# Performance work log

Measured on AMD Instinct MI355X. Metric: run time of the kernel, lower is better.

Reference implementation:

```python
import jax, jax.numpy as jnp
import numpy as np

B, T, U, L, C = 2048, 100, 512, 3, 10


def setup_inputs() -> dict:
    key = jax.random.key(0)
    ks = jax.random.split(key, 2 + 3 * L + 2)
    x = jax.random.normal(ks[0], (B, T, 1), dtype=jnp.float32)
    mask = jax.random.randint(ks[1], (B, T), 0, 2) > 0
    inp = {"x": x, "mask": mask}
    in_dim = 1
    s = 2
    for l in range(L):
        # Keras LSTM kernel layout: gates ordered [i, f, g(candidate), o]
        inp[f"W{l}"] = jax.random.normal(ks[s], (in_dim, 4 * U), dtype=jnp.float32) * 0.05
        inp[f"U{l}"] = jax.random.normal(ks[s + 1], (U, 4 * U), dtype=jnp.float32) * 0.05
        b = np.zeros((4 * U,), dtype=np.float32)
        b[U:2 * U] = 1.0  # unit_forget_bias (Keras default)
        inp[f"b{l}"] = jnp.asarray(b)
        in_dim = U
        s += 2
    inp["Wd"] = jax.random.normal(ks[s], (U, C), dtype=jnp.float32) * 0.05
    inp["bd"] = jnp.zeros((C,), dtype=jnp.float32)
    return inp


def _lstm_step(x_t, h, c, W, Uw, b):
    z = x_t @ W + h @ Uw + b  # [B, 4U]
    i, f, g, o = jnp.split(z, 4, axis=-1)
    i = jax.nn.sigmoid(i)
    f = jax.nn.sigmoid(f)
    g = jnp.tanh(g)
    o = jax.nn.sigmoid(o)
    c_new = f * c + i * g
    h_new = o * jnp.tanh(c_new)
    return h_new, c_new


def reference(x, mask, W0, U0, b0, W1, U1, b1, W2, U2, b2, Wd, bd):
    params = [(W0, U0, b0), (W1, U1, b1), (W2, U2, b2)]
    xt = jnp.swapaxes(x, 0, 1)        # [T, B, 1]
    mt = jnp.swapaxes(mask, 0, 1)     # [T, B]
    Bsz = x.shape[0]
    init = tuple((jnp.zeros((Bsz, U), x.dtype), jnp.zeros((Bsz, U), x.dtype)) for _ in range(L))

    def scan_fn(carry, inp_t):
        x_t, m_t = inp_t
        m = m_t[:, None]  # [B, 1]
        new_states = []
        layer_in = x_t
        for (h, c), (W, Uw, b) in zip(carry, params):
            h_new, c_new = _lstm_step(layer_in, h, c, W, Uw, b)
            # Keras mask semantics: masked steps carry state/output forward
            h_new = jnp.where(m, h_new, h)
            c_new = jnp.where(m, c_new, c)
            new_states.append((h_new, c_new))
            layer_in = h_new
        return tuple(new_states), None

    final, _ = jax.lax.scan(scan_fn, init, (xt, mt))
    h_top = final[-1][0]  # [B, U]
    logits = h_top @ Wd + bd
    return jax.nn.softmax(logits, axis=-1)
```

## Files before the change

### kernel.cpp

```cpp
#include <hip/hip_runtime.h>
#include <cstdint>
#include <cstddef>

#define B_   2048
#define T_   100
#define U_   512
#define NG_  2048
#define C_   10


typedef __attribute__((ext_vector_type(8))) short   short8;
typedef __attribute__((ext_vector_type(4))) float   floatx4;
typedef unsigned short ushort_t;

__device__ inline ushort_t f2bf(float f){
  unsigned u = __float_as_uint(f);
  unsigned r = (u + 0x7FFFu + ((u >> 16) & 1u)) >> 16;
  return (ushort_t)r;
}
__device__ inline float bf2f(ushort_t b){ return __uint_as_float(((unsigned)b) << 16); }

__device__ inline float sigm(float x){ return 1.0f / (1.0f + __expf(-x)); }
__device__ inline float tanh_fast(float x){
  float a = fabsf(x);
  float e = __expf(-2.0f * a);
  float r = (1.0f - e) / (1.0f + e);
  return copysignf(r, x);
}

__device__ inline int orig_col(int p){
  int Tt  = p >> 7;
  int loc = p & 127;
  int half = loc >> 6;
  int loc2 = loc & 63;
  int gate = loc2 >> 4;
  int uu   = (half << 4) | (loc2 & 15);
  return gate * U_ + Tt * 32 + uu;
}

__device__ inline size_t hidx(int b, int u){
  return (((size_t)(b >> 4) * 64 + (size_t)(u >> 3)) * 16 + (b & 15)) * 8 + (u & 7);
}

#define AS1(p) ((const __attribute__((address_space(1))) void*)(p))
#define AS3(p) ((__attribute__((address_space(3))) void*)(p))

__global__ void convert_weights(
    const float* __restrict__ W0, const float* __restrict__ U0, const float* __restrict__ b0,
    const float* __restrict__ W1, const float* __restrict__ U1, const float* __restrict__ b1,
    const float* __restrict__ W2, const float* __restrict__ U2, const float* __restrict__ b2,
    ushort_t* __restrict__ Bt0, ushort_t* __restrict__ Bt1, ushort_t* __restrict__ Bt2,
    float* __restrict__ W0p, float* __restrict__ biasp)
{
  const int N0 = NG_ * 512;
  const int N1 = NG_ * 1024;
  const int total = N0 + 2 * N1 + NG_ + 3 * NG_;
  int idx = blockIdx.x * 256 + threadIdx.x;
  if (idx >= total) return;

  if (idx < N0){
    int p = idx >> 9, k = idx & 511;
    Bt0[idx] = f2bf(U0[(size_t)k * NG_ + orig_col(p)]);
  } else if (idx < N0 + N1){
    int j = idx - N0; int p = j >> 10, k = j & 1023;
    int oc = orig_col(p);
    float v = (k < 512) ? W1[(size_t)k * NG_ + oc] : U1[(size_t)(k - 512) * NG_ + oc];
    Bt1[j] = f2bf(v);
  } else if (idx < N0 + 2 * N1){
    int j = idx - N0 - N1; int p = j >> 10, k = j & 1023;
    int oc = orig_col(p);
    float v = (k < 512) ? W2[(size_t)k * NG_ + oc] : U2[(size_t)(k - 512) * NG_ + oc];
    Bt2[j] = f2bf(v);
  } else if (idx < N0 + 2 * N1 + NG_){
    int p = idx - N0 - 2 * N1;
    W0p[p] = W0[orig_col(p)];
  } else {
    int j = idx - N0 - 2 * N1 - NG_;
    int l = j >> 11, p = j & 2047;
    const float* bs = (l == 0) ? b0 : (l == 1) ? b1 : b2;
    biasp[j] = bs[orig_col(p)];
  }
}

template<int LAYER>
__device__ __forceinline__ void do_task(
    const ushort_t* __restrict__ A0,
    const ushort_t* __restrict__ A1,
    const ushort_t* __restrict__ Bt,
    const float* __restrict__ biasp,
    const float* __restrict__ W0p,
    const float* __restrict__ x,
    const int* __restrict__ mask,
    float* __restrict__ cbuf,
    const ushort_t* __restrict__ hprev,
    ushort_t* __restrict__ hout,
    int t, int mt, int nt,
    ushort_t* tB)
{
  constexpr int NPHASE = (LAYER == 0) ? 1 : 2;
  constexpr bool IS_L0 = (LAYER == 0);
  constexpr int K  = NPHASE * 512;
  constexpr int NK = NPHASE * 8;

  const int tid  = threadIdx.x;
  const int wv   = tid >> 6;
  const int lane = tid & 63;
  const int qd   = lane >> 4;
  const int l16  = lane & 15;
  const int wave_m = wv >> 1;
  const int wave_n = wv & 1;
  const int m0 = mt * 128, n0 = nt * 128;

  int srow[4], scol[4];
  #pragma unroll
  for (int cc = 0; cc < 4; ++cc){
    int i = cc * 256 + tid;
    srow[cc] = i >> 3;
    scol[cc] = ((i & 7) + (i >> 3)) & 7;
  }

  int boff[2][4];
  #pragma unroll
  for (int ks = 0; ks < 2; ++ks){
    #pragma unroll
    for (int w = 0; w < 4; ++w){
      int Rb = wave_n * 64 + w * 16 + l16;
      int q  = ks * 4 + qd;
      boff[ks][w] = Rb * 64 + ((q - Rb) & 7) * 8;
    }
  }

  size_t abase[4];
  #pragma unroll
  for (int wm = 0; wm < 4; ++wm)
    abase[wm] = ((size_t)((m0 >> 4) + wave_m * 4 + wm)) * 8192
              + (size_t)qd * 128 + (size_t)l16 * 8;

  floatx4 acc[4][4];
  #pragma unroll
  for (int i = 0; i < 4; ++i)
    #pragma unroll
    for (int j = 0; j < 4; ++j) acc[i][j] = (floatx4){0.f, 0.f, 0.f, 0.f};

  auto stageB = [&](int kk, int buf){
    const int phh = kk >> 3;
    const int kk0 = (kk & 7) << 6;
    ushort_t* dst = tB + buf * 8192;
    #pragma unroll
    for (int cc = 0; cc < 4; ++cc){
      const int ibase = cc * 256 + wv * 64;
      const ushort_t* gb = Bt + (size_t)(n0 + srow[cc]) * K + phh * 512 + kk0 + scol[cc] * 8;
      __builtin_amdgcn_global_load_lds(AS1(gb), AS3(&dst[ibase * 8]), 16, 0, 0);
    }
  };

  stageB(0, 0);
  __syncthreads();

  int cur = 0;
  for (int kk = 0; kk < NK; ++kk){
    const int k0 = (kk & 7) << 6;
    const ushort_t* A = (NPHASE == 2 && kk >= 8) ? A1 : A0;

    short8 af[2][4];
    #pragma unroll
    for (int ks = 0; ks < 2; ++ks)
      #pragma unroll
      for (int wm = 0; wm < 4; ++wm)
        af[ks][wm] = *(const short8*)&A[abase[wm] + (size_t)(k0 * 16 + ks * 512)];

    if (kk + 1 < NK) stageB(kk + 1, cur ^ 1);

    const ushort_t* tb = tB + cur * 8192;
    #pragma unroll
    for (int ks = 0; ks < 2; ++ks){
      short8 bfr[4];
      #pragma unroll
      for (int wn = 0; wn < 4; ++wn)
        bfr[wn] = *(const short8*)&tb[boff[ks][wn]];
      #pragma unroll
      for (int wm = 0; wm < 4; ++wm)
        #pragma unroll
        for (int wn = 0; wn < 4; ++wn)
          acc[wm][wn] = __builtin_amdgcn_mfma_f32_16x16x32_bf16(af[ks][wm], bfr[wn], acc[wm][wn], 0, 0, 0);
    }
    __syncthreads();
    cur ^= 1;
  }

  const int u  = nt * 32 + wave_n * 16 + l16;
  const int pb = nt * 128 + wave_n * 64 + l16;
  const float bi = biasp[pb], bf_ = biasp[pb + 16], bg = biasp[pb + 32], bo = biasp[pb + 48];
  float wi = 0.f, wf = 0.f, wg = 0.f, wo = 0.f;
  if (IS_L0){ wi = W0p[pb]; wf = W0p[pb + 16]; wg = W0p[pb + 32]; wo = W0p[pb + 48]; }

  #pragma unroll
  for (int wm = 0; wm < 4; ++wm){
    #pragma unroll
    for (int reg = 0; reg < 4; ++reg){
      int b = m0 + wave_m * 64 + wm * 16 + qd * 4 + reg;
      float zi = acc[wm][0][reg] + bi;
      float zf = acc[wm][1][reg] + bf_;
      float zg = acc[wm][2][reg] + bg;
      float zo = acc[wm][3][reg] + bo;
      if (IS_L0){
        float xv = x[(size_t)b * T_ + t];
        zi += xv * wi; zf += xv * wf; zg += xv * wg; zo += xv * wo;
      }
      int mk = mask[(size_t)b * T_ + t];
      size_t su = (size_t)b * U_ + u;
      size_t sf = hidx(b, u);
      float c_old = cbuf[su];
      float i_ = sigm(zi), f_ = sigm(zf), g_ = tanh_fast(zg), o_ = sigm(zo);
      float c_new = f_ * c_old + i_ * g_;
      float h_new = o_ * tanh_fast(c_new);
      ushort_t hb = mk ? f2bf(h_new) : hprev[sf];
      cbuf[su] = mk ? c_new : c_old;
      hout[sf] = hb;
    }
  }
}

__global__ __launch_bounds__(256, 3) void lstm_phase(
    const ushort_t* __restrict__ Bt0, const ushort_t* __restrict__ Bt1,
    const ushort_t* __restrict__ Bt2, const float* __restrict__ biasp,
    const float* __restrict__ W0p, const float* __restrict__ x,
    const int* __restrict__ mask,
    ushort_t* h00, ushort_t* h01, ushort_t* h10, ushort_t* h11,
    ushort_t* h20, ushort_t* h21,
    float* c0, float* c1, float* c2,
    int s)
{
  __shared__ __align__(16) ushort_t tB[2 * 128 * 64];

  const int lin  = blockIdx.x;
  const int task = lin >> 8;
  const int tile = lin & 255;
  const int mt = tile >> 4, nt = tile & 15;

  ushort_t* h0[2] = {h00, h01};
  ushort_t* h1[2] = {h10, h11};
  ushort_t* h2[2] = {h20, h21};

  if (task == 0){
    if (s >= 100) return;
    int t = s, p = t & 1;
    do_task<0>(h0[p], nullptr, Bt0, biasp, W0p, x, mask,
               c0, h0[p], h0[p ^ 1], t, mt, nt, tB);
  } else if (task == 1){
    if (s < 1 || s > 100) return;
    int t = s - 1, p = t & 1;
    do_task<1>(h0[p ^ 1], h1[p], Bt1, biasp + NG_, nullptr, x, mask,
               c1, h1[p], h1[p ^ 1], t, mt, nt, tB);
  } else {
    if (s < 2) return;
    int t = s - 2, p = t & 1;
    do_task<2>(h1[p ^ 1], h2[p], Bt2, biasp + 2 * NG_, nullptr, x, mask,
               c2, h2[p], h2[p ^ 1], t, mt, nt, tB);
  }
}

__global__ __launch_bounds__(256) void head_softmax(
    const ushort_t* __restrict__ h2, const float* __restrict__ Wd,
    const float* __restrict__ bd, float* __restrict__ out)
{
  int wv = threadIdx.x >> 6, lane = threadIdx.x & 63;
  int row = blockIdx.x * 4 + wv;
  const ushort_t* hr = h2 + (((size_t)(row >> 4) * 64 + lane) * 16 + (row & 15)) * 8;

  float acc[C_];
  #pragma unroll
  for (int c = 0; c < C_; ++c) acc[c] = 0.f;

  short8 hv = *(const short8*)hr;
  #pragma unroll
  for (int j = 0; j < 8; ++j){
    float hf = bf2f((ushort_t)hv[j]);
    int k = lane * 8 + j;
    #pragma unroll
    for (int c = 0; c < C_; ++c) acc[c] += hf * Wd[k * C_ + c];
  }
  #pragma unroll
  for (int c = 0; c < C_; ++c){
    float v = acc[c];
    #pragma unroll
    for (int off = 32; off > 0; off >>= 1) v += __shfl_xor(v, off);
    acc[c] = v + bd[c];
  }
  float mx = acc[0];
  #pragma unroll
  for (int c = 1; c < C_; ++c) mx = fmaxf(mx, acc[c]);
  float e[C_]; float s = 0.f;
  #pragma unroll
  for (int c = 0; c < C_; ++c){ e[c] = __expf(acc[c] - mx); s += e[c]; }
  float inv = 1.0f / s;
  if (lane == 0){
    #pragma unroll
    for (int c = 0; c < C_; ++c) out[(size_t)row * C_ + c] = e[c] * inv;
  }
}

extern "C" void kernel_launch(void* const* d_in, const int* in_sizes, int n_in,
                              void* d_out, int out_size, void* d_ws, size_t ws_size,
                              hipStream_t stream)
{
  const float* x  = (const float*)d_in[0];
  const int*  mask= (const int*)  d_in[1];
  const float* W0 = (const float*)d_in[2];
  const float* U0 = (const float*)d_in[3];
  const float* b0 = (const float*)d_in[4];
  const float* W1 = (const float*)d_in[5];
  const float* U1 = (const float*)d_in[6];
  const float* b1 = (const float*)d_in[7];
  const float* W2 = (const float*)d_in[8];
  const float* U2 = (const float*)d_in[9];
  const float* b2 = (const float*)d_in[10];
  const float* Wd = (const float*)d_in[11];
  const float* bd = (const float*)d_in[12];
  float* out = (float*)d_out;

  char* ws = (char*)d_ws;
  size_t off = 0;
  auto alloc = [&](size_t sz) -> char* {
    char* p = ws + off; off = (off + sz + 255) & ~(size_t)255; return p;
  };
  ushort_t* Bt0  = (ushort_t*)alloc((size_t)NG_ * 512 * 2);
  ushort_t* Bt1  = (ushort_t*)alloc((size_t)NG_ * 1024 * 2);
  ushort_t* Bt2  = (ushort_t*)alloc((size_t)NG_ * 1024 * 2);
  float*    W0p  = (float*)alloc((size_t)NG_ * 4);
  float*    biasp= (float*)alloc((size_t)3 * NG_ * 4);

  const size_t hsz = (size_t)B_ * U_ * 2;
  const size_t csz = (size_t)B_ * U_ * 4;
  char* state = alloc(6 * hsz + 3 * csz);
  ushort_t* hb[3][2]; float* cb[3];
  {
    char* pp = state;
    for (int l = 0; l < 3; ++l)
      for (int par = 0; par < 2; ++par){ hb[l][par] = (ushort_t*)pp; pp += hsz; }
    for (int l = 0; l < 3; ++l){ cb[l] = (float*)pp; pp += csz; }
  }

  hipMemsetAsync(state, 0, 6 * hsz + 3 * csz, stream);

  const int total = NG_ * 512 + 2 * NG_ * 1024 + NG_ + 3 * NG_;
  convert_weights<<<(total + 255) / 256, 256, 0, stream>>>(
      W0, U0, b0, W1, U1, b1, W2, U2, b2, Bt0, Bt1, Bt2, W0p, biasp);

  for (int s = 0; s < 102; ++s){
    lstm_phase<<<768, 256, 0, stream>>>(
        Bt0, Bt1, Bt2, biasp, W0p, x, mask,
        hb[0][0], hb[0][1], hb[1][0], hb[1][1], hb[2][0], hb[2][1],
        cb[0], cb[1], cb[2], s);
  }

  head_softmax<<<B_ / 4, 256, 0, stream>>>(hb[2][0], Wd, bd, out);
}
```

Baseline: 4.146 ms.

## Pre-swizzle weights into MFMA fragment order and stage activations through LDS

Weights are reordered at conversion time into per-wave MFMA B-fragment order, so each wave reads its B operands directly from global memory with contiguous 16-byte loads. The hidden-state activations are now stored row-major and staged into LDS through double-buffered global_load_lds, replacing the swizzled per-fragment A layout that was read directly from global. The intent is to cut LDS traffic and bank conflicts for the larger operand and to simplify the state layout. In exchange, B loads now go straight from global or L2 on every k-step with no LDS reuse across the tile's waves, and the A staging plus barriers stay on the critical path.

```diff
diff --git a/kernel.cpp b/kernel.cpp
--- a/kernel.cpp
+++ b/kernel.cpp
@@ -38,10 +38,6 @@
   return gate * U_ + Tt * 32 + uu;
 }
 
-__device__ inline size_t hidx(int b, int u){
-  return (((size_t)(b >> 4) * 64 + (size_t)(u >> 3)) * 16 + (b & 15)) * 8 + (u & 7);
-}
-
 #define AS1(p) ((const __attribute__((address_space(1))) void*)(p))
 #define AS3(p) ((__attribute__((address_space(3))) void*)(p))
 
@@ -49,7 +45,7 @@
     const float* __restrict__ W0, const float* __restrict__ U0, const float* __restrict__ b0,
     const float* __restrict__ W1, const float* __restrict__ U1, const float* __restrict__ b1,
     const float* __restrict__ W2, const float* __restrict__ U2, const float* __restrict__ b2,
-    ushort_t* __restrict__ Bt0, ushort_t* __restrict__ Bt1, ushort_t* __restrict__ Bt2,
+    ushort_t* __restrict__ Bf0, ushort_t* __restrict__ Bf1, ushort_t* __restrict__ Bf2,
     float* __restrict__ W0p, float* __restrict__ biasp)
 {
   const int N0 = NG_ * 512;
@@ -59,18 +55,25 @@
   if (idx >= total) return;
 
   if (idx < N0){
-    int p = idx >> 9, k = idx & 511;
-    Bt0[idx] = f2bf(U0[(size_t)k * NG_ + orig_col(p)]);
-  } else if (idx < N0 + N1){
-    int j = idx - N0; int p = j >> 10, k = j & 1023;
+    int i = idx;
+    int j = i & 7, l = (i >> 3) & 63, wn = (i >> 9) & 3;
+    int ks = (i >> 11) & 15, w = (i >> 15) & 1, nt = i >> 16;
+    int p = nt * 128 + w * 64 + wn * 16 + (l & 15);
+    int k = ks * 32 + ((l >> 4) << 3) + j;
+    Bf0[i] = f2bf(U0[(size_t)k * NG_ + orig_col(p)]);
+  } else if (idx < N0 + 2 * N1){
+    int seg = (idx - N0) / N1;
+    int i = (idx - N0) - seg * N1;
+    int j = i & 7, l = (i >> 3) & 63, wn = (i >> 9) & 3;
+    int ks = (i >> 11) & 31, w = (i >> 16) & 1, nt = i >> 17;
+    int p = nt * 128 + w * 64 + wn * 16 + (l & 15);
+    int k = ks * 32 + ((l >> 4) << 3) + j;
     int oc = orig_col(p);
-    float v = (k < 512) ? W1[(size_t)k * NG_ + oc] : U1[(size_t)(k - 512) * NG_ + oc];
-    Bt1[j] = f2bf(v);
-  } else if (idx < N0 + 2 * N1){
-    int j = idx - N0 - N1; int p = j >> 10, k = j & 1023;
-    int oc = orig_col(p);
-    float v = (k < 512) ? W2[(size_t)k * NG_ + oc] : U2[(size_t)(k - 512) * NG_ + oc];
-    Bt2[j] = f2bf(v);
+    const float* Wl = (seg == 0) ? W1 : W2;
+    const float* Ul = (seg == 0) ? U1 : U2;
+    float v = (k < 512) ? Wl[(size_t)k * NG_ + oc] : Ul[(size_t)(k - 512) * NG_ + oc];
+    ushort_t* Bf = (seg == 0) ? Bf1 : Bf2;
+    Bf[i] = f2bf(v);
   } else if (idx < N0 + 2 * N1 + NG_){
     int p = idx - N0 - 2 * N1;
     W0p[p] = W0[orig_col(p)];
@@ -86,7 +89,7 @@
 __device__ __forceinline__ void do_task(
     const ushort_t* __restrict__ A0,
     const ushort_t* __restrict__ A1,
-    const ushort_t* __restrict__ Bt,
+    const ushort_t* __restrict__ Bf,
     const float* __restrict__ biasp,
     const float* __restrict__ W0p,
     const float* __restrict__ x,
@@ -95,7 +98,7 @@
     const ushort_t* __restrict__ hprev,
     ushort_t* __restrict__ hout,
     int t, int mt, int nt,
-    ushort_t* tB)
+    ushort_t* tA)
 {
   constexpr int NPHASE = (LAYER == 0) ? 1 : 2;
   constexpr bool IS_L0 = (LAYER == 0);
@@ -119,22 +122,18 @@
     scol[cc] = ((i & 7) + (i >> 3)) & 7;
   }
 
-  int boff[2][4];
+  int aoff[2][4];
   #pragma unroll
   for (int ks = 0; ks < 2; ++ks){
     #pragma unroll
     for (int w = 0; w < 4; ++w){
-      int Rb = wave_n * 64 + w * 16 + l16;
+      int Ra = wave_m * 64 + w * 16 + l16;
       int q  = ks * 4 + qd;
-      boff[ks][w] = Rb * 64 + ((q - Rb) & 7) * 8;
+      aoff[ks][w] = Ra * 64 + ((q - Ra) & 7) * 8;
     }
   }
 
-  size_t abase[4];
-  #pragma unroll
-  for (int wm = 0; wm < 4; ++wm)
-    abase[wm] = ((size_t)((m0 >> 4) + wave_m * 4 + wm)) * 8192
-              + (size_t)qd * 128 + (size_t)l16 * 8;
+  const ushort_t* Bw = Bf + (size_t)(nt * 2 + wave_n) * ((size_t)K * 64) + lane * 8;
 
   floatx4 acc[4][4];
   #pragma unroll
@@ -142,50 +141,49 @@
     #pragma unroll
     for (int j = 0; j < 4; ++j) acc[i][j] = (floatx4){0.f, 0.f, 0.f, 0.f};
 
-  auto stageB = [&](int kk, int buf){
-    const int phh = kk >> 3;
-    const int kk0 = (kk & 7) << 6;
-    ushort_t* dst = tB + buf * 8192;
+  auto stageA = [&](int kk, int b){
+    const ushort_t* A = (NPHASE == 2 && kk >= 8) ? A1 : A0;
+    const int k0 = (kk & 7) << 6;
+    ushort_t* dst = tA + b * 8192;
     #pragma unroll
     for (int cc = 0; cc < 4; ++cc){
       const int ibase = cc * 256 + wv * 64;
-      const ushort_t* gb = Bt + (size_t)(n0 + srow[cc]) * K + phh * 512 + kk0 + scol[cc] * 8;
-      __builtin_amdgcn_global_load_lds(AS1(gb), AS3(&dst[ibase * 8]), 16, 0, 0);
+      const ushort_t* ga = A + (size_t)(m0 + srow[cc]) * U_ + k0 + scol[cc] * 8;
+      __builtin_amdgcn_global_load_lds(AS1(ga), AS3(&dst[ibase * 8]), 16, 0, 0);
     }
   };
 
-  stageB(0, 0);
+  stageA(0, 0);
   __syncthreads();
 
-  int cur = 0;
   for (int kk = 0; kk < NK; ++kk){
-    const int k0 = (kk & 7) << 6;
-    const ushort_t* A = (NPHASE == 2 && kk >= 8) ? A1 : A0;
-
+    if (kk + 1 < NK) stageA(kk + 1, (kk + 1) & 1);
+
+    const ushort_t* bkk = Bw + (size_t)kk * 4096;
+    short8 bfr[2][4];
+    #pragma unroll
+    for (int ks = 0; ks < 2; ++ks)
+      #pragma unroll
+      for (int wn = 0; wn < 4; ++wn)
+        bfr[ks][wn] = *(const short8*)&bkk[ks * 2048 + wn * 512];
+
+    const ushort_t* ta = tA + (kk & 1) * 8192;
     short8 af[2][4];
     #pragma unroll
     for (int ks = 0; ks < 2; ++ks)
       #pragma unroll
       for (int wm = 0; wm < 4; ++wm)
-        af[ks][wm] = *(const short8*)&A[abase[wm] + (size_t)(k0 * 16 + ks * 512)];
-
-    if (kk + 1 < NK) stageB(kk + 1, cur ^ 1);
-
-    const ushort_t* tb = tB + cur * 8192;
-    #pragma unroll
-    for (int ks = 0; ks < 2; ++ks){
-      short8 bfr[4];
-      #pragma unroll
-      for (int wn = 0; wn < 4; ++wn)
-        bfr[wn] = *(const short8*)&tb[boff[ks][wn]];
+        af[ks][wm] = *(const short8*)&ta[aoff[ks][wm]];
+
+    #pragma unroll
+    for (int ks = 0; ks < 2; ++ks)
       #pragma unroll
       for (int wm = 0; wm < 4; ++wm)
         #pragma unroll
         for (int wn = 0; wn < 4; ++wn)
-          acc[wm][wn] = __builtin_amdgcn_mfma_f32_16x16x32_bf16(af[ks][wm], bfr[wn], acc[wm][wn], 0, 0, 0);
-    }
+          acc[wm][wn] = __builtin_amdgcn_mfma_f32_16x16x32_bf16(af[ks][wm], bfr[ks][wn], acc[wm][wn], 0, 0, 0);
+
     __syncthreads();
-    cur ^= 1;
   }
 
   const int u  = nt * 32 + wave_n * 16 + l16;
@@ -209,21 +207,20 @@
       }
       int mk = mask[(size_t)b * T_ + t];
       size_t su = (size_t)b * U_ + u;
-      size_t sf = hidx(b, u);
       float c_old = cbuf[su];
       float i_ = sigm(zi), f_ = sigm(zf), g_ = tanh_fast(zg), o_ = sigm(zo);
       float c_new = f_ * c_old + i_ * g_;
       float h_new = o_ * tanh_fast(c_new);
-      ushort_t hb = mk ? f2bf(h_new) : hprev[sf];
+      ushort_t hb = mk ? f2bf(h_new) : hprev[su];
       cbuf[su] = mk ? c_new : c_old;
-      hout[sf] = hb;
+      hout[su] = hb;
     }
   }
 }
 
 __global__ __launch_bounds__(256, 3) void lstm_phase(
-    const ushort_t* __restrict__ Bt0, const ushort_t* __restrict__ Bt1,
-    const ushort_t* __restrict__ Bt2, const float* __restrict__ biasp,
+    const ushort_t* __restrict__ Bf0, const ushort_t* __restrict__ Bf1,
+    const ushort_t* __restrict__ Bf2, const float* __restrict__ biasp,
     const float* __restrict__ W0p, const float* __restrict__ x,
     const int* __restrict__ mask,
     ushort_t* h00, ushort_t* h01, ushort_t* h10, ushort_t* h11,
@@ -231,7 +228,7 @@
     float* c0, float* c1, float* c2,
     int s)
 {
-  __shared__ __align__(16) ushort_t tB[2 * 128 * 64];
+  __shared__ __align__(16) ushort_t tA[2 * 128 * 64];
 
   const int lin  = blockIdx.x;
   const int task = lin >> 8;
@@ -245,18 +242,18 @@
   if (task == 0){
     if (s >= 100) return;
     int t = s, p = t & 1;
-    do_task<0>(h0[p], nullptr, Bt0, biasp, W0p, x, mask,
-               c0, h0[p], h0[p ^ 1], t, mt, nt, tB);
+    do_task<0>(h0[p], nullptr, Bf0, biasp, W0p, x, mask,
+               c0, h0[p], h0[p ^ 1], t, mt, nt, tA);
   } else if (task == 1){
     if (s < 1 || s > 100) return;
     int t = s - 1, p = t & 1;
-    do_task<1>(h0[p ^ 1], h1[p], Bt1, biasp + NG_, nullptr, x, mask,
-               c1, h1[p], h1[p ^ 1], t, mt, nt, tB);
+    do_task<1>(h0[p ^ 1], h1[p], Bf1, biasp + NG_, nullptr, x, mask,
+               c1, h1[p], h1[p ^ 1], t, mt, nt, tA);
   } else {
     if (s < 2) return;
     int t = s - 2, p = t & 1;
-    do_task<2>(h1[p ^ 1], h2[p], Bt2, biasp + 2 * NG_, nullptr, x, mask,
-               c2, h2[p], h2[p ^ 1], t, mt, nt, tB);
+    do_task<2>(h1[p ^ 1], h2[p], Bf2, biasp + 2 * NG_, nullptr, x, mask,
+               c2, h2[p], h2[p ^ 1], t, mt, nt, tA);
   }
 }
 
@@ -266,13 +263,13 @@
 {
   int wv = threadIdx.x >> 6, lane = threadIdx.x & 63;
   int row = blockIdx.x * 4 + wv;
-  const ushort_t* hr = h2 + (((size_t)(row >> 4) * 64 + lane) * 16 + (row & 15)) * 8;
+  const ushort_t* hr = h2 + (size_t)row * U_;
 
   float acc[C_];
   #pragma unroll
   for (int c = 0; c < C_; ++c) acc[c] = 0.f;
 
-  short8 hv = *(const short8*)hr;
+  short8 hv = *(const short8*)&hr[lane * 8];
   #pragma unroll
   for (int j = 0; j < 8; ++j){
     float hf = bf2f((ushort_t)hv[j]);
@@ -324,9 +321,9 @@
   auto alloc = [&](size_t sz) -> char* {
     char* p = ws + off; off = (off + sz + 255) & ~(size_t)255; return p;
   };
-  ushort_t* Bt0  = (ushort_t*)alloc((size_t)NG_ * 512 * 2);
-  ushort_t* Bt1  = (ushort_t*)alloc((size_t)NG_ * 1024 * 2);
-  ushort_t* Bt2  = (ushort_t*)alloc((size_t)NG_ * 1024 * 2);
+  ushort_t* Bf0  = (ushort_t*)alloc((size_t)NG_ * 512 * 2);
+  ushort_t* Bf1  = (ushort_t*)alloc((size_t)NG_ * 1024 * 2);
+  ushort_t* Bf2  = (ushort_t*)alloc((size_t)NG_ * 1024 * 2);
   float*    W0p  = (float*)alloc((size_t)NG_ * 4);
   float*    biasp= (float*)alloc((size_t)3 * NG_ * 4);
 
@@ -345,11 +342,11 @@
 
   const int total = NG_ * 512 + 2 * NG_ * 1024 + NG_ + 3 * NG_;
   convert_weights<<<(total + 255) / 256, 256, 0, stream>>>(
-      W0, U0, b0, W1, U1, b1, W2, U2, b2, Bt0, Bt1, Bt2, W0p, biasp);
+      W0, U0, b0, W1, U1, b1, W2, U2, b2, Bf0, Bf1, Bf2, W0p, biasp);
 
   for (int s = 0; s < 102; ++s){
     lstm_phase<<<768, 256, 0, stream>>>(
-        Bt0, Bt1, Bt2, biasp, W0p, x, mask,
+        Bf0, Bf1, Bf2, biasp, W0p, x, mask,
         hb[0][0], hb[0][1], hb[1][0], hb[1][1], hb[2][0], hb[2][1],
         cb[0], cb[1], cb[2], s);
   }
```

Result: faster. 3.839 ms (-7.4%).
